# Performance work log

Hardware: AMD Instinct MI355X
Metric: run time of the kernel (lower is better)

Reference implementation:

```python
import jax, jax.numpy as jnp
import numpy as np

EPS = 1e-5
EMBED_DIM = 1024
CTX_DIM = 768
NUM_HEADS = 16
DH = EMBED_DIM // NUM_HEADS
# Faithful to torch source: embed_dim // num_heads ** 0.5 parses as embed_dim // (num_heads**0.5)
SCALE = EMBED_DIM // (NUM_HEADS ** 0.5)  # = 256.0


def ws_conv1x1(x, w, b, mask):
    # weight-standardized 1x1 conv1d: w [O, I, 1], x [B, I, T]
    w2 = w[..., 0]
    mu = jnp.mean(w2, axis=1, keepdims=True)
    var = jnp.var(w2, axis=1, keepdims=True)
    wn = (w2 - mu) * jax.lax.rsqrt(var + EPS)
    y = jnp.einsum('oi,bit->bot', wn, x) + b[None, :, None]
    if mask is not None:
        y = jnp.where(mask, y, 0.0)  # mask [B,1,T] bool
    return y


def layernorm(x, g, b):
    # normalize over last axis
    mu = jnp.mean(x, axis=-1, keepdims=True)
    var = jnp.var(x, axis=-1, keepdims=True)
    return (x - mu) * jax.lax.rsqrt(var + EPS) * g + b


def setup_inputs() -> dict:
    key = jax.random.key(0)
    ks = jax.random.split(key, 16)
    B, T, S = 4, 1024, 1024
    inp = {
        'x': jax.random.normal(ks[0], (B, EMBED_DIM, T), dtype=jnp.float32),
        'context': jax.random.normal(ks[1], (B, CTX_DIM, S), dtype=jnp.float32),
        'mask': jax.random.randint(ks[2], (B, 1, T), 0, 2).astype(bool),
        'mask_ctx': jax.random.randint(ks[3], (B, 1, S), 0, 2).astype(bool),
        'qw': jax.random.normal(ks[4], (EMBED_DIM, EMBED_DIM, 1), dtype=jnp.float32) * 0.02,
        'qb': jnp.zeros((EMBED_DIM,), jnp.float32),
        'kw': jax.random.normal(ks[5], (EMBED_DIM, CTX_DIM, 1), dtype=jnp.float32) * 0.02,
        'kb': jnp.zeros((EMBED_DIM,), jnp.float32),
        'vw': jax.random.normal(ks[6], (EMBED_DIM, CTX_DIM, 1), dtype=jnp.float32) * 0.02,
        'vb': jnp.zeros((EMBED_DIM,), jnp.float32),
        'ow': jax.random.normal(ks[7], (EMBED_DIM, EMBED_DIM, 1), dtype=jnp.float32) * 0.02,
        'ob': jnp.zeros((EMBED_DIM,), jnp.float32),
        'gq': jnp.ones((DH,), jnp.float32), 'bq': jnp.zeros((DH,), jnp.float32),
        'gk': jnp.ones((DH,), jnp.float32), 'bk': jnp.zeros((DH,), jnp.float32),
        'gv': jnp.ones((DH,), jnp.float32), 'bv': jnp.zeros((DH,), jnp.float32),
    }
    return inp


def reference(x, context, mask, mask_ctx, qw, qb, kw, kb, vw, vb, ow, ob, gq, bq, gk, bk, gv, bv):
    B, E, T = x.shape
    S = context.shape[-1]
    q = ws_conv1x1(x, qw, qb, mask)            # [B,E,T]
    k = ws_conv1x1(context, kw, kb, mask_ctx)  # [B,E,S]
    v = ws_conv1x1(context, vw, vb, mask_ctx)  # [B,E,S]
    # split heads -> [B,H,dh,L]
    q = q.reshape(B, NUM_HEADS, DH, T)
    k = k.reshape(B, NUM_HEADS, DH, S)
    v = v.reshape(B, NUM_HEADS, DH, S)
    # middle_norm: LayerNorm over dh (applied on transposed layout)
    q = jnp.swapaxes(layernorm(jnp.swapaxes(q, -1, -2), gq, bq), -1, -2)
    k = jnp.swapaxes(layernorm(jnp.swapaxes(k, -1, -2), gk, bk), -1, -2)
    v = jnp.swapaxes(layernorm(jnp.swapaxes(v, -1, -2), gv, bv), -1, -2)
    # scores: k^T @ q -> [B,H,S,T]
    scores = jnp.einsum('bhds,bhdt->bhst', k, q) / SCALE
    scores = jnp.where(mask[:, :, None, :], scores, -1e9)  # mask over query dim T
    scores = jax.nn.softmax(scores, axis=-1)               # softmax over T (as in source)
    scores = jnp.where(mask_ctx[:, :, :, None], scores, 0.0)
    out = jnp.einsum('bhds,bhst->bhdt', v, scores)          # v @ scores -> [B,H,dh,T]
    out = out.reshape(B, E, T)
    out = ws_conv1x1(out, ow, ob, mask) + x
    return out
```

## Files before the change

### kernel.cpp

```cpp
#include <hip/hip_runtime.h>

#define NB 4
#define TT 1024
#define SS 1024
#define EE 1024
#define CCH 768
#define NH 16
#define DHH 64
#define EPSF 1e-5f
#define QSCALE (1.4426950408889634f / 256.0f)

typedef unsigned short u16;
typedef __attribute__((ext_vector_type(8))) short short8;
typedef __attribute__((ext_vector_type(8))) unsigned short u16x8;
typedef __attribute__((ext_vector_type(4))) unsigned short u16x4;
typedef __attribute__((ext_vector_type(4))) float f32x4;

__device__ __forceinline__ u16 f2bu(float f) {
    union { float f; unsigned u; } x; x.f = f;
    unsigned r = x.u + 0x7fffu + ((x.u >> 16) & 1u);
    return (u16)(r >> 16);
}
__device__ __forceinline__ float bu2f(u16 u) {
    union { unsigned u; float f; } x; x.u = ((unsigned)u) << 16; return x.f;
}

#if __has_builtin(__builtin_amdgcn_exp2f)
#define EXP2(x) __builtin_amdgcn_exp2f(x)
#else
#define EXP2(x) exp2f(x)
#endif

#define MFMA16(a, b, c) __builtin_amdgcn_mfma_f32_16x16x32_bf16((a), (b), (c), 0, 0, 0)

__device__ __forceinline__ void gload16(const void* g, void* l) {
    __builtin_amdgcn_global_load_lds(
        (const __attribute__((address_space(1))) void*)g,
        (__attribute__((address_space(3))) void*)l, 16, 0, 0);
}

template<int R>
__device__ __forceinline__ void stage_tile(
    const u16* __restrict__ g, int ldg, u16* lds, int w, int lane) {
    constexpr int PW = R / 32;
    int r0 = lane >> 3;
    int cs = ((lane & 7) << 4) ^ (r0 << 4);
#pragma unroll
    for (int j = 0; j < PW; j++) {
        int inst = w * PW + j;
        const u16* src = g + (size_t)(inst * 8 + r0) * ldg + (cs >> 1);
        gload16(src, lds + inst * 512);
    }
}

__device__ __forceinline__ const u16* swz_ptr(const u16* tile, int row, int col) {
    int off = row * 128 + ((col * 2) ^ ((row & 7) << 4));
    return (const u16*)((const char*)tile + off);
}

#define PREP_WS_END   4096
#define PREP_SCAN_END (PREP_WS_END + 8)
#define PREP_TR_END   (PREP_SCAN_END + 1792)
#define PREP_FILL_END (PREP_TR_END + 4096)

__global__ __launch_bounds__(256) void prep(
    const float* __restrict__ qw, const float* __restrict__ kw,
    const float* __restrict__ vw, const float* __restrict__ ow,
    u16* __restrict__ wqn, u16* __restrict__ wkn,
    u16* __restrict__ wvn, u16* __restrict__ won,
    const float* __restrict__ x, const float* __restrict__ ctx,
    const int* __restrict__ mask, const int* __restrict__ mask_ctx,
    u16* __restrict__ xc, u16* __restrict__ cc,
    int* __restrict__ tIdx, int* __restrict__ sIdx,
    int* __restrict__ cntQ, int* __restrict__ cntK,
    float* __restrict__ outF) {
    __shared__ float tile[64][65];
    __shared__ int spos[64], smask[64], wtoti[4];
    __shared__ float sa[4], sb2[4], smean, srstd;
    int bid = blockIdx.x, tid = threadIdx.x;

    if (bid < PREP_WS_END) {
        int mat = bid >> 10, row = bid & 1023;
        const float* w = mat == 0 ? qw : (mat == 1 ? kw : (mat == 2 ? vw : ow));
        u16* wn = mat == 0 ? wqn : (mat == 1 ? wkn : (mat == 2 ? wvn : won));
        int I = (mat == 1 || mat == 2) ? CCH : EE;
        const float* wr = w + (size_t)row * I;
        int nv = I >> 8;
        float vals[4];
        float s = 0.f, s2 = 0.f;
        for (int j = 0; j < nv; j++) {
            float v = wr[tid + 256 * j];
            vals[j] = v; s += v; s2 += v * v;
        }
#pragma unroll
        for (int off = 32; off > 0; off >>= 1) { s += __shfl_down(s, off); s2 += __shfl_down(s2, off); }
        int wid = tid >> 6;
        if ((tid & 63) == 0) { sa[wid] = s; sb2[wid] = s2; }
        __syncthreads();
        if (tid == 0) {
            float ts = sa[0] + sa[1] + sa[2] + sa[3];
            float ts2 = sb2[0] + sb2[1] + sb2[2] + sb2[3];
            float mean = ts / (float)I;
            float var = ts2 / (float)I - mean * mean;
            smean = mean; srstd = rsqrtf(var + EPSF);
        }
        __syncthreads();
        float mean = smean, r = srstd;
        u16* wo = wn + (size_t)row * I;
        for (int j = 0; j < nv; j++) wo[tid + 256 * j] = f2bu((vals[j] - mean) * r);
        return;
    }
    if (bid < PREP_SCAN_END) {
        int t = bid - PREP_WS_END;
        int which = t & 1, b = t >> 1;
        const int* m = (which ? mask_ctx : mask) + b * 1024;
        int* idx = (which ? sIdx : tIdx) + b * 1024;
        int* cnt = (which ? cntK : cntQ) + b;
        int base = tid * 4;
        int v[4]; int s = 0;
#pragma unroll
        for (int i = 0; i < 4; i++) { v[i] = m[base + i] ? 1 : 0; s += v[i]; }
        int lane = tid & 63, wid = tid >> 6;
        int inc = s;
#pragma unroll
        for (int off = 1; off < 64; off <<= 1) {
            int o = __shfl_up(inc, off);
            if (lane >= off) inc += o;
        }
        if (lane == 63) wtoti[wid] = inc;
        __syncthreads();
        int woff = 0;
        for (int i = 0; i < wid; i++) woff += wtoti[i];
        int p = woff + inc - s;
#pragma unroll
        for (int i = 0; i < 4; i++) {
            if (v[i]) idx[p] = base + i;
            p += v[i];
        }
        if (tid == 255) *cnt = p;
        return;
    }
    if (bid < PREP_TR_END) {
        int t = bid - PREP_SCAN_END;
        int xb = t & 15; int rem = t >> 4;
        int yy = rem % 28, b = rem / 28;
        int mat = yy < 16 ? 0 : 1;
        int r0 = (mat == 0 ? yy : yy - 16) * 64;
        int R = mat == 0 ? EE : CCH;
        const float* in = mat == 0 ? x : ctx;
        const int* m = (mat == 0 ? mask : mask_ctx) + (size_t)b * 1024;
        u16* out = mat == 0 ? xc : cc;
        int c0 = xb * 64;
        const float* ip = in + (size_t)b * R * 1024;
        u16* op = out + (size_t)b * R * 1024;
#pragma unroll
        for (int mm = 0; mm < 16; mm++) {
            int id = tid + 256 * mm; int r = id >> 6, c = id & 63;
            tile[r][c] = ip[(size_t)(r0 + r) * 1024 + c0 + c];
        }
        int base = tid * 4;
        int v[4]; int s = 0;
#pragma unroll
        for (int i = 0; i < 4; i++) { v[i] = m[base + i] ? 1 : 0; s += v[i]; }
        int lane = tid & 63, wid = tid >> 6;
        int inc = s;
#pragma unroll
        for (int off = 1; off < 64; off <<= 1) {
            int o = __shfl_up(inc, off);
            if (lane >= off) inc += o;
        }
        if (lane == 63) wtoti[wid] = inc;
        __syncthreads();
        int woff = 0;
        for (int i = 0; i < wid; i++) woff += wtoti[i];
        int p = woff + inc - s;
#pragma unroll
        for (int i = 0; i < 4; i++) {
            int g = base + i;
            if (g >= c0 && g < c0 + 64) { spos[g - c0] = p; smask[g - c0] = v[i]; }
            p += v[i];
        }
        __syncthreads();
#pragma unroll
        for (int mm = 0; mm < 16; mm++) {
            int id = tid + 256 * mm; int rr = id >> 6, cc2 = id & 63;
            if (smask[rr])
                op[(size_t)spos[rr] * R + r0 + cc2] = f2bu(tile[cc2][rr]);
        }
        return;
    }
    {
        int f = bid - PREP_TR_END;
        int b = f >> 10, o = f & 1023;
        const float* xr = x + ((size_t)b * EE + o) * TT;
        float* orow = outF + ((size_t)b * EE + o) * TT;
        const int* mrow = mask + (size_t)b * TT;
        int4 mv = ((const int4*)mrow)[tid];
        float4 xv = ((const float4*)xr)[tid];
        int t4 = tid * 4;
        if (!mv.x) orow[t4 + 0] = xv.x;
        if (!mv.y) orow[t4 + 1] = xv.y;
        if (!mv.z) orow[t4 + 2] = xv.z;
        if (!mv.w) orow[t4 + 3] = xv.w;
    }
}

__device__ __forceinline__ void gemm_core(
    const u16* __restrict__ A, const u16* __restrict__ Bp, int I,
    int o0, int l0, u16 (*at)[128][64], u16 (*bt)[64][64], f32x4 (&acc)[4][2]) {
    int tid = threadIdx.x;
    int w = tid >> 6, lane = tid & 63, quad = lane >> 4, l16 = lane & 15;
    int wm = w & 1, wn = w >> 1;
    const u16* Ab = A + (size_t)o0 * I;
    const u16* Bb = Bp + (size_t)l0 * I;
    stage_tile<128>(Ab, I, &at[0][0][0], w, lane);
    stage_tile<64>(Bb, I, &bt[0][0][0], w, lane);
    __syncthreads();
    int cur = 0;
    for (int k0 = 0; k0 < I; k0 += 64, cur ^= 1) {
        int kn = k0 + 64;
        if (kn < I) {
            stage_tile<128>(Ab + kn, I, &at[cur ^ 1][0][0], w, lane);
            stage_tile<64>(Bb + kn, I, &bt[cur ^ 1][0][0], w, lane);
        }
#pragma unroll
        for (int ks = 0; ks < 64; ks += 32) {
            short8 af[4], bf[2];
#pragma unroll
            for (int i = 0; i < 4; i++)
                af[i] = *(const short8*)swz_ptr(&at[cur][0][0], wm * 64 + i * 16 + l16, ks + quad * 8);
#pragma unroll
            for (int j = 0; j < 2; j++)
                bf[j] = *(const short8*)swz_ptr(&bt[cur][0][0], wn * 32 + j * 16 + l16, ks + quad * 8);
#pragma unroll
            for (int mt = 0; mt < 4; mt++)
#pragma unroll
                for (int nt = 0; nt < 2; nt++)
                    acc[mt][nt] = MFMA16(af[mt], bf[nt], acc[mt][nt]);
        }
        __syncthreads();
    }
}

__global__ __launch_bounds__(256) void proj_qkv(
    const u16* __restrict__ wq, const u16* __restrict__ wk, const u16* __restrict__ wv,
    const u16* __restrict__ xc, const u16* __restrict__ cc,
    const float* __restrict__ qb, const float* __restrict__ kb, const float* __restrict__ vbi,
    const int* __restrict__ cntQ, const int* __restrict__ cntK,
    const float* __restrict__ gq, const float* __restrict__ bq,
    const float* __restrict__ gk, const float* __restrict__ bk,
    const float* __restrict__ gv, const float* __restrict__ bv,
    u16* __restrict__ qc, u16* __restrict__ kc, u16* __restrict__ vn) {
    int mat = blockIdx.x >> 3;
    int o0 = (blockIdx.x & 7) * 128;
    int l0 = blockIdx.y * 64;
    int b = blockIdx.z;
    int limit = (mat == 0) ? cntQ[b] : cntK[b];
    if (l0 >= limit) return;
    __shared__ u16 at[2][128][64];
    __shared__ u16 bt[2][64][64];
    __shared__ float sg[64], sbe[64], sbias[128];
    int tid = threadIdx.x;
    int w = tid >> 6, lane = tid & 63, quad = lane >> 4, l16 = lane & 15;
    int wm = w & 1, wn = w >> 1;
    const u16* A = mat == 0 ? wq : (mat == 1 ? wk : wv);
    const u16* BT = mat == 0 ? xc : cc;
    const float* bias = mat == 0 ? qb : (mat == 1 ? kb : vbi);
    int I = mat == 0 ? EE : CCH;
    if (tid < 64) {
        const float* gsrc = mat == 0 ? gq : (mat == 1 ? gk : gv);
        const float* bsrc = mat == 0 ? bq : (mat == 1 ? bk : bv);
        sg[tid] = gsrc[tid];
        sbe[tid] = bsrc[tid];
    }
    if (tid < 128) sbias[tid] = bias[o0 + tid];

    f32x4 acc[4][2] = {};
    gemm_core(A, BT + (size_t)b * 1024 * I, I, o0, l0, at, bt, acc);

    float scale = mat == 0 ? QSCALE : 1.0f;
    int h = (o0 >> 6) + wm;
    int bh = b * NH + h;
#pragma unroll
    for (int nt = 0; nt < 2; nt++) {
        int l = l0 + wn * 32 + nt * 16 + l16;
        float vbuf[16];
        float s = 0.f;
#pragma unroll
        for (int mt = 0; mt < 4; mt++)
#pragma unroll
            for (int reg = 0; reg < 4; reg++) {
                float v = acc[mt][nt][reg] + sbias[wm * 64 + mt * 16 + quad * 4 + reg];
                vbuf[mt * 4 + reg] = v; s += v;
            }
        s += __shfl_xor(s, 16); s += __shfl_xor(s, 32);
        float mean = s * (1.f / 64);
        float s2 = 0.f;
#pragma unroll
        for (int i = 0; i < 16; i++) { float dv = vbuf[i] - mean; s2 += dv * dv; }
        s2 += __shfl_xor(s2, 16); s2 += __shfl_xor(s2, 32);
        float r = rsqrtf(s2 * (1.f / 64) + EPSF);
        if (l < limit) {
            if (mat < 2) {
                u16* outT = mat == 0 ? qc : kc;
                u16* op = outT + ((size_t)bh * 1024 + l) * 64;
#pragma unroll
                for (int mt = 0; mt < 4; mt++) {
                    u16x4 pk;
#pragma unroll
                    for (int reg = 0; reg < 4; reg++) {
                        int d = mt * 16 + quad * 4 + reg;
                        pk[reg] = f2bu(((vbuf[mt * 4 + reg] - mean) * r * sg[d] + sbe[d]) * scale);
                    }
                    *(u16x4*)&op[mt * 16 + quad * 4] = pk;
                }
            } else {
#pragma unroll
                for (int mt = 0; mt < 4; mt++)
#pragma unroll
                    for (int reg = 0; reg < 4; reg++) {
                        int d = mt * 16 + quad * 4 + reg;
                        vn[((size_t)b * EE + h * 64 + d) * 1024 + l] =
                            f2bu((vbuf[mt * 4 + reg] - mean) * r * sg[d] + sbe[d]);
                    }
            }
        }
    }
}

__global__ __launch_bounds__(256) void attn_stats_mfma(
    const u16* __restrict__ qc, const u16* __restrict__ kc,
    const int* __restrict__ cntQ, const int* __restrict__ cntK,
    u16* __restrict__ vn, u16* __restrict__ P) {
    int s0 = blockIdx.x * 64, h = blockIdx.y, b = blockIdx.z;
    int Sc = cntK[b], Tc = cntQ[b];
    if (s0 >= Sc) return;
    __shared__ u16 kt[64][64];
    __shared__ u16 qt[2][64][64];
    __shared__ float lp[4][64];
    int tid = threadIdx.x;
    int w = tid >> 6, lane = tid & 63, quad = lane >> 4, l16 = lane & 15;
    int head = b * NH + h;
    const u16* kp = kc + (size_t)head * SS * DHH;
    const u16* qp = qc + (size_t)head * TT * DHH;
    u16* Pb = P + (size_t)head * TT * SS;
    stage_tile<64>(kp + (size_t)s0 * DHH, DHH, &kt[0][0], w, lane);
    stage_tile<64>(qp, DHH, &qt[0][0][0], w, lane);
    __syncthreads();
    float rl[4][4] = {};
    int cur = 0;
    for (int t0 = 0; t0 < Tc; t0 += 64, cur ^= 1) {
        if (t0 + 64 < Tc)
            stage_tile<64>(qp + (size_t)(t0 + 64) * DHH, DHH, &qt[cur ^ 1][0][0], w, lane);
        f32x4 acc[4] = {};
#pragma unroll
        for (int ks = 0; ks < 64; ks += 32) {
            short8 bf = *(const short8*)swz_ptr(&qt[cur][0][0], w * 16 + l16, ks + quad * 8);
#pragma unroll
            for (int mt = 0; mt < 4; mt++) {
                short8 af = *(const short8*)swz_ptr(&kt[0][0], mt * 16 + l16, ks + quad * 8);
                acc[mt] = MFMA16(af, bf, acc[mt]);
            }
        }
        int tcol = t0 + w * 16 + l16;
        int tok = tcol < Tc;
#pragma unroll
        for (int mt = 0; mt < 4; mt++) {
            u16x4 pk;
#pragma unroll
            for (int reg = 0; reg < 4; reg++) {
                int sl = s0 + mt * 16 + quad * 4 + reg;
                float e = EXP2(acc[mt][reg]);
                if (tok) rl[mt][reg] += e;
                pk[reg] = (sl < Sc) ? f2bu(e) : (u16)0;
            }
            *(u16x4*)&Pb[(size_t)tcol * SS + s0 + mt * 16 + quad * 4] = pk;
        }
        __syncthreads();
    }
#pragma unroll
    for (int mt = 0; mt < 4; mt++) {
#pragma unroll
        for (int reg = 0; reg < 4; reg++) {
            float v = rl[mt][reg];
            v += __shfl_xor(v, 1); v += __shfl_xor(v, 2);
            v += __shfl_xor(v, 4); v += __shfl_xor(v, 8);
            if (l16 == 0) lp[w][mt * 16 + quad * 4 + reg] = v;
        }
    }
    __syncthreads();
    {
        int so = tid & 63, dg = tid >> 6;
        int s = s0 + so;
        float lv = lp[0][so] + lp[1][so] + lp[2][so] + lp[3][so];
        float wsc = (lv > 0.f) ? (1.f / lv) : 0.f;
        u16* vrow = vn + ((size_t)b * EE + h * 64) * SS;
        int live = s < Sc;
#pragma unroll
        for (int i = 0; i < 16; i++) {
            int d = dg * 16 + i;
            size_t a = (size_t)d * SS + s;
            vrow[a] = live ? f2bu(bu2f(vrow[a]) * wsc) : (u16)0;
        }
    }
}

__global__ __launch_bounds__(256) void attn_pv_mfma(
    const u16* __restrict__ vn, const u16* __restrict__ P,
    const int* __restrict__ cntQ, const int* __restrict__ cntK,
    u16* __restrict__ ac) {
    int t0 = blockIdx.x * 64, h = blockIdx.y, b = blockIdx.z;
    int Tc = cntQ[b], Sc = cntK[b];
    if (t0 >= Tc) return;
    int Kc = (Sc + 63) & ~63;
    __shared__ u16 at[2][64][64];
    __shared__ u16 bt[2][64][64];
    __shared__ u16 pt[64][72];
    int tid = threadIdx.x;
    int w = tid >> 6, lane = tid & 63, quad = lane >> 4, l16 = lane & 15;
    int head = b * NH + h;
    const u16* vp = vn + ((size_t)head * DHH) * SS;
    const u16* Pb = P + (size_t)head * TT * SS + (size_t)t0 * SS;
    f32x4 oacc[4] = {};
    if (Kc > 0) {
        stage_tile<64>(vp, SS, &at[0][0][0], w, lane);
        stage_tile<64>(Pb, SS, &bt[0][0][0], w, lane);
        __syncthreads();
        int cur = 0;
        for (int k0 = 0; k0 < Kc; k0 += 64, cur ^= 1) {
            int kn = k0 + 64;
            if (kn < Kc) {
                stage_tile<64>(vp + kn, SS, &at[cur ^ 1][0][0], w, lane);
                stage_tile<64>(Pb + kn, SS, &bt[cur ^ 1][0][0], w, lane);
            }
#pragma unroll
            for (int ks = 0; ks < 64; ks += 32) {
                short8 bf = *(const short8*)swz_ptr(&bt[cur][0][0], w * 16 + l16, ks + quad * 8);
#pragma unroll
                for (int mt = 0; mt < 4; mt++) {
                    short8 af = *(const short8*)swz_ptr(&at[cur][0][0], mt * 16 + l16, ks + quad * 8);
                    oacc[mt] = MFMA16(af, bf, oacc[mt]);
                }
            }
            __syncthreads();
        }
    }
    int tl = w * 16 + l16;
#pragma unroll
    for (int mt = 0; mt < 4; mt++) {
        u16x4 pk;
#pragma unroll
        for (int reg = 0; reg < 4; reg++) pk[reg] = f2bu(oacc[mt][reg]);
        *(u16x4*)&pt[tl][mt * 16 + quad * 4] = pk;
    }
    __syncthreads();
#pragma unroll
    for (int i = 0; i < 2; i++) {
        int id = tid * 2 + i;
        int r = id >> 3, c = (id & 7) * 8;
        if (t0 + r < Tc)
            *(u16x8*)&ac[((size_t)b * TT + t0 + r) * EE + h * 64 + c] =
                *(const u16x8*)&pt[r][c];
    }
}

__global__ __launch_bounds__(256) void proj_o(
    const u16* __restrict__ won, const u16* __restrict__ ac,
    const float* __restrict__ obi, const int* __restrict__ tIdx,
    const int* __restrict__ cntQ, const float* __restrict__ x,
    float* __restrict__ out) {
    int o0 = blockIdx.x * 128, l0 = blockIdx.y * 64, b = blockIdx.z;
    int Tc = cntQ[b];
    if (l0 >= Tc) return;
    __shared__ u16 at[2][128][64];
    __shared__ u16 bt[2][64][64];
    __shared__ float sbias[128];
    __shared__ int stre[64];
    int tid = threadIdx.x;
    int w = tid >> 6, lane = tid & 63, quad = lane >> 4, l16 = lane & 15;
    int wm = w & 1, wn = w >> 1;
    if (tid < 128) sbias[tid] = obi[o0 + tid];
    if (tid < 64) stre[tid] = tIdx[(size_t)b * 1024 + l0 + tid];
    f32x4 acc[4][2] = {};
    gemm_core(won, ac + (size_t)b * TT * EE, EE, o0, l0, at, bt, acc);
#pragma unroll
    for (int nt = 0; nt < 2; nt++) {
        int lcol = wn * 32 + nt * 16 + l16;
        int l = l0 + lcol;
        if (l < Tc) {
            int treal = stre[lcol];
#pragma unroll
            for (int mt = 0; mt < 4; mt++)
#pragma unroll
                for (int reg = 0; reg < 4; reg++) {
                    int o = o0 + wm * 64 + mt * 16 + quad * 4 + reg;
                    size_t off = ((size_t)b * EE + o) * TT + treal;
                    out[off] = acc[mt][nt][reg] + sbias[wm * 64 + mt * 16 + quad * 4 + reg] + x[off];
                }
        }
    }
}

extern "C" void kernel_launch(void* const* d_in, const int* in_sizes, int n_in,
                              void* d_out, int out_size, void* d_ws, size_t ws_size,
                              hipStream_t stream) {
    const float* x        = (const float*)d_in[0];
    const float* ctx      = (const float*)d_in[1];
    const int*   mask     = (const int*)d_in[2];
    const int*   mask_ctx = (const int*)d_in[3];
    const float* qw  = (const float*)d_in[4];
    const float* qbi = (const float*)d_in[5];
    const float* kw  = (const float*)d_in[6];
    const float* kbi = (const float*)d_in[7];
    const float* vw  = (const float*)d_in[8];
    const float* vbi = (const float*)d_in[9];
    const float* ow  = (const float*)d_in[10];
    const float* obi = (const float*)d_in[11];
    const float* gq = (const float*)d_in[12];
    const float* bq = (const float*)d_in[13];
    const float* gk = (const float*)d_in[14];
    const float* bk = (const float*)d_in[15];
    const float* gv = (const float*)d_in[16];
    const float* bv = (const float*)d_in[17];

    u16* p = (u16*)d_ws;
    u16* wqn = p; p += (size_t)EE * EE;
    u16* wkn = p; p += (size_t)EE * CCH;
    u16* wvn = p; p += (size_t)EE * CCH;
    u16* won = p; p += (size_t)EE * EE;
    u16* xc  = p; p += (size_t)NB * TT * EE;
    u16* cc  = p; p += (size_t)NB * SS * CCH;
    u16* vn  = p; p += (size_t)NB * EE * SS;
    u16* qc  = p; p += (size_t)NB * NH * TT * DHH;
    u16* kc  = p; p += (size_t)NB * NH * SS * DHH;
    u16* ac  = p; p += (size_t)NB * TT * EE;
    u16* P   = p; p += (size_t)NB * NH * TT * SS;
    int* tIdx = (int*)p;
    int* sIdx = tIdx + NB * 1024;
    int* cntQ = sIdx + NB * 1024;
    int* cntK = cntQ + NB;

    prep<<<PREP_FILL_END, 256, 0, stream>>>(
        qw, kw, vw, ow, wqn, wkn, wvn, won, x, ctx, mask, mask_ctx,
        xc, cc, tIdx, sIdx, cntQ, cntK, (float*)d_out);

    proj_qkv<<<dim3(24, 16, NB), 256, 0, stream>>>(
        wqn, wkn, wvn, xc, cc, qbi, kbi, vbi, cntQ, cntK,
        gq, bq, gk, bk, gv, bv, qc, kc, vn);

    attn_stats_mfma<<<dim3(16, NH, NB), 256, 0, stream>>>(
        qc, kc, cntQ, cntK, vn, P);

    attn_pv_mfma<<<dim3(16, NH, NB), 256, 0, stream>>>(
        vn, P, cntQ, cntK, ac);

    proj_o<<<dim3(8, 16, NB), 256, 0, stream>>>(
        won, ac, obi, tIdx, cntQ, x, (float*)d_out);
}
```

Before: 227.1 us.

## Fuse attention stats, PV and output projection into one persistent kernel with grid barriers

Replaces three separate kernel launches (attention scores/exp, P·V, output projection) with a single kernel of 1024 blocks that runs the three phases back to back, separated by software grid barriers built on atomic counters. Shared memory is unioned across phases, and the output projection is retiled from 128x64 to 64x64 so it maps onto the same 1024-block grid. The goal is to remove launch gaps and tail effects between stages. In exchange it relies on all 1024 blocks being co-resident (launch bounds of 4 blocks per CU), pays for atomic spin barriers, and gives up the larger projection tile's data reuse.

```diff
diff --git a/kernel.cpp b/kernel.cpp
--- a/kernel.cpp
+++ b/kernel.cpp
@@ -10,6 +10,8 @@
 #define EPSF 1e-5f
 #define QSCALE (1.4426950408889634f / 256.0f)
 
+#define ATTN_BLKS 1024
+
 typedef unsigned short u16;
 typedef __attribute__((ext_vector_type(8))) short short8;
 typedef __attribute__((ext_vector_type(8))) unsigned short u16x8;
@@ -32,6 +34,21 @@
 #endif
 
 #define MFMA16(a, b, c) __builtin_amdgcn_mfma_f32_16x16x32_bf16((a), (b), (c), 0, 0, 0)
+
+__device__ unsigned int g_cnt[4];
+
+__device__ __forceinline__ void grid_barrier(int idx) {
+    __syncthreads();
+    if (threadIdx.x == 0) {
+        __threadfence();
+        unsigned ticket = atomicAdd(&g_cnt[idx], 1u);
+        unsigned target = (ticket / ATTN_BLKS + 1u) * ATTN_BLKS;
+        while (atomicAdd(&g_cnt[idx], 0u) < target)
+            __builtin_amdgcn_s_sleep(2);
+        __threadfence();
+    }
+    __syncthreads();
+}
 
 __device__ __forceinline__ void gload16(const void* g, void* l) {
     __builtin_amdgcn_global_load_lds(
@@ -328,175 +345,203 @@
     }
 }
 
-__global__ __launch_bounds__(256) void attn_stats_mfma(
+union ASMem {
+    struct {
+        u16 kt[64][64];
+        u16 qt[2][64][64];
+        float lp[4][64];
+    } st;
+    struct {
+        u16 at[2][64][64];
+        u16 bt[2][64][64];
+    } pv;
+    struct {
+        u16 at[2][64][64];
+        u16 bt[2][64][64];
+        float sbias[64];
+        int stre[64];
+    } po;
+};
+
+__global__ __launch_bounds__(256, 4) void attn_all(
     const u16* __restrict__ qc, const u16* __restrict__ kc,
+    u16* __restrict__ vn, u16* __restrict__ P, u16* __restrict__ ac,
+    const u16* __restrict__ won, const float* __restrict__ obi,
+    const int* __restrict__ tIdx,
     const int* __restrict__ cntQ, const int* __restrict__ cntK,
-    u16* __restrict__ vn, u16* __restrict__ P) {
-    int s0 = blockIdx.x * 64, h = blockIdx.y, b = blockIdx.z;
-    int Sc = cntK[b], Tc = cntQ[b];
-    if (s0 >= Sc) return;
-    __shared__ u16 kt[64][64];
-    __shared__ u16 qt[2][64][64];
-    __shared__ float lp[4][64];
-    int tid = threadIdx.x;
+    const float* __restrict__ x, float* __restrict__ out) {
+    __shared__ ASMem sm;
+    int bid = blockIdx.x, tid = threadIdx.x;
     int w = tid >> 6, lane = tid & 63, quad = lane >> 4, l16 = lane & 15;
-    int head = b * NH + h;
-    const u16* kp = kc + (size_t)head * SS * DHH;
-    const u16* qp = qc + (size_t)head * TT * DHH;
-    u16* Pb = P + (size_t)head * TT * SS;
-    stage_tile<64>(kp + (size_t)s0 * DHH, DHH, &kt[0][0], w, lane);
-    stage_tile<64>(qp, DHH, &qt[0][0][0], w, lane);
-    __syncthreads();
-    float rl[4][4] = {};
-    int cur = 0;
-    for (int t0 = 0; t0 < Tc; t0 += 64, cur ^= 1) {
-        if (t0 + 64 < Tc)
-            stage_tile<64>(qp + (size_t)(t0 + 64) * DHH, DHH, &qt[cur ^ 1][0][0], w, lane);
-        f32x4 acc[4] = {};
-#pragma unroll
-        for (int ks = 0; ks < 64; ks += 32) {
-            short8 bf = *(const short8*)swz_ptr(&qt[cur][0][0], w * 16 + l16, ks + quad * 8);
+    int gx = bid & 15, gy = (bid >> 4) & 15, b = bid >> 8;
+
+    {
+        int s0 = gx * 64, h = gy;
+        int Sc = cntK[b], Tc = cntQ[b];
+        if (s0 < Sc) {
+            int head = b * NH + h;
+            const u16* kp = kc + (size_t)head * SS * DHH;
+            const u16* qp = qc + (size_t)head * TT * DHH;
+            u16* Pb = P + (size_t)head * TT * SS;
+            stage_tile<64>(kp + (size_t)s0 * DHH, DHH, &sm.st.kt[0][0], w, lane);
+            stage_tile<64>(qp, DHH, &sm.st.qt[0][0][0], w, lane);
+            __syncthreads();
+            float rl[4][4] = {};
+            int cur = 0;
+            for (int t0 = 0; t0 < Tc; t0 += 64, cur ^= 1) {
+                if (t0 + 64 < Tc)
+                    stage_tile<64>(qp + (size_t)(t0 + 64) * DHH, DHH, &sm.st.qt[cur ^ 1][0][0], w, lane);
+                f32x4 acc[4] = {};
+#pragma unroll
+                for (int ks = 0; ks < 64; ks += 32) {
+                    short8 bf = *(const short8*)swz_ptr(&sm.st.qt[cur][0][0], w * 16 + l16, ks + quad * 8);
+#pragma unroll
+                    for (int mt = 0; mt < 4; mt++) {
+                        short8 af = *(const short8*)swz_ptr(&sm.st.kt[0][0], mt * 16 + l16, ks + quad * 8);
+                        acc[mt] = MFMA16(af, bf, acc[mt]);
+                    }
+                }
+                int tcol = t0 + w * 16 + l16;
+                int tok = tcol < Tc;
+#pragma unroll
+                for (int mt = 0; mt < 4; mt++) {
+                    u16x4 pk;
+#pragma unroll
+                    for (int reg = 0; reg < 4; reg++) {
+                        int sl = s0 + mt * 16 + quad * 4 + reg;
+                        float e = EXP2(acc[mt][reg]);
+                        if (tok) rl[mt][reg] += e;
+                        pk[reg] = (sl < Sc) ? f2bu(e) : (u16)0;
+                    }
+                    *(u16x4*)&Pb[(size_t)tcol * SS + s0 + mt * 16 + quad * 4] = pk;
+                }
+                __syncthreads();
+            }
 #pragma unroll
             for (int mt = 0; mt < 4; mt++) {
-                short8 af = *(const short8*)swz_ptr(&kt[0][0], mt * 16 + l16, ks + quad * 8);
-                acc[mt] = MFMA16(af, bf, acc[mt]);
-            }
-        }
-        int tcol = t0 + w * 16 + l16;
-        int tok = tcol < Tc;
-#pragma unroll
-        for (int mt = 0; mt < 4; mt++) {
-            u16x4 pk;
-#pragma unroll
-            for (int reg = 0; reg < 4; reg++) {
-                int sl = s0 + mt * 16 + quad * 4 + reg;
-                float e = EXP2(acc[mt][reg]);
-                if (tok) rl[mt][reg] += e;
-                pk[reg] = (sl < Sc) ? f2bu(e) : (u16)0;
-            }
-            *(u16x4*)&Pb[(size_t)tcol * SS + s0 + mt * 16 + quad * 4] = pk;
-        }
-        __syncthreads();
-    }
-#pragma unroll
-    for (int mt = 0; mt < 4; mt++) {
-#pragma unroll
-        for (int reg = 0; reg < 4; reg++) {
-            float v = rl[mt][reg];
-            v += __shfl_xor(v, 1); v += __shfl_xor(v, 2);
-            v += __shfl_xor(v, 4); v += __shfl_xor(v, 8);
-            if (l16 == 0) lp[w][mt * 16 + quad * 4 + reg] = v;
-        }
-    }
-    __syncthreads();
+#pragma unroll
+                for (int reg = 0; reg < 4; reg++) {
+                    float v = rl[mt][reg];
+                    v += __shfl_xor(v, 1); v += __shfl_xor(v, 2);
+                    v += __shfl_xor(v, 4); v += __shfl_xor(v, 8);
+                    if (l16 == 0) sm.st.lp[w][mt * 16 + quad * 4 + reg] = v;
+                }
+            }
+            __syncthreads();
+            {
+                int so = tid & 63, dg = tid >> 6;
+                int s = s0 + so;
+                float lv = sm.st.lp[0][so] + sm.st.lp[1][so] + sm.st.lp[2][so] + sm.st.lp[3][so];
+                float wsc = (lv > 0.f) ? (1.f / lv) : 0.f;
+                u16* vrow = vn + ((size_t)b * EE + h * 64) * SS;
+                int live = s < Sc;
+#pragma unroll
+                for (int i = 0; i < 16; i++) {
+                    int d = dg * 16 + i;
+                    size_t ad = (size_t)d * SS + s;
+                    vrow[ad] = live ? f2bu(bu2f(vrow[ad]) * wsc) : (u16)0;
+                }
+            }
+        }
+    }
+    grid_barrier(0);
     {
-        int so = tid & 63, dg = tid >> 6;
-        int s = s0 + so;
-        float lv = lp[0][so] + lp[1][so] + lp[2][so] + lp[3][so];
-        float wsc = (lv > 0.f) ? (1.f / lv) : 0.f;
-        u16* vrow = vn + ((size_t)b * EE + h * 64) * SS;
-        int live = s < Sc;
-#pragma unroll
-        for (int i = 0; i < 16; i++) {
-            int d = dg * 16 + i;
-            size_t a = (size_t)d * SS + s;
-            vrow[a] = live ? f2bu(bu2f(vrow[a]) * wsc) : (u16)0;
-        }
-    }
-}
-
-__global__ __launch_bounds__(256) void attn_pv_mfma(
-    const u16* __restrict__ vn, const u16* __restrict__ P,
-    const int* __restrict__ cntQ, const int* __restrict__ cntK,
-    u16* __restrict__ ac) {
-    int t0 = blockIdx.x * 64, h = blockIdx.y, b = blockIdx.z;
-    int Tc = cntQ[b], Sc = cntK[b];
-    if (t0 >= Tc) return;
-    int Kc = (Sc + 63) & ~63;
-    __shared__ u16 at[2][64][64];
-    __shared__ u16 bt[2][64][64];
-    __shared__ u16 pt[64][72];
-    int tid = threadIdx.x;
-    int w = tid >> 6, lane = tid & 63, quad = lane >> 4, l16 = lane & 15;
-    int head = b * NH + h;
-    const u16* vp = vn + ((size_t)head * DHH) * SS;
-    const u16* Pb = P + (size_t)head * TT * SS + (size_t)t0 * SS;
-    f32x4 oacc[4] = {};
-    if (Kc > 0) {
-        stage_tile<64>(vp, SS, &at[0][0][0], w, lane);
-        stage_tile<64>(Pb, SS, &bt[0][0][0], w, lane);
-        __syncthreads();
-        int cur = 0;
-        for (int k0 = 0; k0 < Kc; k0 += 64, cur ^= 1) {
-            int kn = k0 + 64;
-            if (kn < Kc) {
-                stage_tile<64>(vp + kn, SS, &at[cur ^ 1][0][0], w, lane);
-                stage_tile<64>(Pb + kn, SS, &bt[cur ^ 1][0][0], w, lane);
-            }
-#pragma unroll
-            for (int ks = 0; ks < 64; ks += 32) {
-                short8 bf = *(const short8*)swz_ptr(&bt[cur][0][0], w * 16 + l16, ks + quad * 8);
-#pragma unroll
-                for (int mt = 0; mt < 4; mt++) {
-                    short8 af = *(const short8*)swz_ptr(&at[cur][0][0], mt * 16 + l16, ks + quad * 8);
-                    oacc[mt] = MFMA16(af, bf, oacc[mt]);
-                }
+        int t0 = gx * 64, h = gy;
+        int Tc = cntQ[b], Sc = cntK[b];
+        if (t0 < Tc) {
+            int Kc = (Sc + 63) & ~63;
+            int head = b * NH + h;
+            const u16* vp = vn + ((size_t)head * DHH) * SS;
+            const u16* Pb = P + (size_t)head * TT * SS + (size_t)t0 * SS;
+            f32x4 oacc[4] = {};
+            if (Kc > 0) {
+                stage_tile<64>(vp, SS, &sm.pv.at[0][0][0], w, lane);
+                stage_tile<64>(Pb, SS, &sm.pv.bt[0][0][0], w, lane);
+                __syncthreads();
+                int cur = 0;
+                for (int k0 = 0; k0 < Kc; k0 += 64, cur ^= 1) {
+                    int kn = k0 + 64;
+                    if (kn < Kc) {
+                        stage_tile<64>(vp + kn, SS, &sm.pv.at[cur ^ 1][0][0], w, lane);
+                        stage_tile<64>(Pb + kn, SS, &sm.pv.bt[cur ^ 1][0][0], w, lane);
+                    }
+#pragma unroll
+                    for (int ks = 0; ks < 64; ks += 32) {
+                        short8 bf = *(const short8*)swz_ptr(&sm.pv.bt[cur][0][0], w * 16 + l16, ks + quad * 8);
+#pragma unroll
+                        for (int mt = 0; mt < 4; mt++) {
+                            short8 af = *(const short8*)swz_ptr(&sm.pv.at[cur][0][0], mt * 16 + l16, ks + quad * 8);
+                            oacc[mt] = MFMA16(af, bf, oacc[mt]);
+                        }
+                    }
+                    __syncthreads();
+                }
+            }
+            u16 (*pt)[72] = (u16(*)[72])&sm.pv.at[0][0][0];
+            int tl = w * 16 + l16;
+#pragma unroll
+            for (int mt = 0; mt < 4; mt++) {
+                u16x4 pk;
+#pragma unroll
+                for (int reg = 0; reg < 4; reg++) pk[reg] = f2bu(oacc[mt][reg]);
+                *(u16x4*)&pt[tl][mt * 16 + quad * 4] = pk;
             }
             __syncthreads();
-        }
-    }
-    int tl = w * 16 + l16;
-#pragma unroll
-    for (int mt = 0; mt < 4; mt++) {
-        u16x4 pk;
-#pragma unroll
-        for (int reg = 0; reg < 4; reg++) pk[reg] = f2bu(oacc[mt][reg]);
-        *(u16x4*)&pt[tl][mt * 16 + quad * 4] = pk;
-    }
-    __syncthreads();
-#pragma unroll
-    for (int i = 0; i < 2; i++) {
-        int id = tid * 2 + i;
-        int r = id >> 3, c = (id & 7) * 8;
-        if (t0 + r < Tc)
-            *(u16x8*)&ac[((size_t)b * TT + t0 + r) * EE + h * 64 + c] =
-                *(const u16x8*)&pt[r][c];
-    }
-}
-
-__global__ __launch_bounds__(256) void proj_o(
-    const u16* __restrict__ won, const u16* __restrict__ ac,
-    const float* __restrict__ obi, const int* __restrict__ tIdx,
-    const int* __restrict__ cntQ, const float* __restrict__ x,
-    float* __restrict__ out) {
-    int o0 = blockIdx.x * 128, l0 = blockIdx.y * 64, b = blockIdx.z;
-    int Tc = cntQ[b];
-    if (l0 >= Tc) return;
-    __shared__ u16 at[2][128][64];
-    __shared__ u16 bt[2][64][64];
-    __shared__ float sbias[128];
-    __shared__ int stre[64];
-    int tid = threadIdx.x;
-    int w = tid >> 6, lane = tid & 63, quad = lane >> 4, l16 = lane & 15;
-    int wm = w & 1, wn = w >> 1;
-    if (tid < 128) sbias[tid] = obi[o0 + tid];
-    if (tid < 64) stre[tid] = tIdx[(size_t)b * 1024 + l0 + tid];
-    f32x4 acc[4][2] = {};
-    gemm_core(won, ac + (size_t)b * TT * EE, EE, o0, l0, at, bt, acc);
-#pragma unroll
-    for (int nt = 0; nt < 2; nt++) {
-        int lcol = wn * 32 + nt * 16 + l16;
-        int l = l0 + lcol;
-        if (l < Tc) {
-            int treal = stre[lcol];
-#pragma unroll
-            for (int mt = 0; mt < 4; mt++)
-#pragma unroll
-                for (int reg = 0; reg < 4; reg++) {
-                    int o = o0 + wm * 64 + mt * 16 + quad * 4 + reg;
-                    size_t off = ((size_t)b * EE + o) * TT + treal;
-                    out[off] = acc[mt][nt][reg] + sbias[wm * 64 + mt * 16 + quad * 4 + reg] + x[off];
-                }
+#pragma unroll
+            for (int i = 0; i < 2; i++) {
+                int id = tid * 2 + i;
+                int r = id >> 3, c = (id & 7) * 8;
+                if (t0 + r < Tc)
+                    *(u16x8*)&ac[((size_t)b * TT + t0 + r) * EE + gy * 64 + c] =
+                        *(const u16x8*)&pt[r][c];
+            }
+        }
+    }
+    grid_barrier(1);
+    {
+        int o0 = gx * 64, l0 = gy * 64;
+        int Tc = cntQ[b];
+        if (l0 < Tc) {
+            if (tid < 64) {
+                sm.po.sbias[tid] = obi[o0 + tid];
+                sm.po.stre[tid] = tIdx[(size_t)b * 1024 + l0 + tid];
+            }
+            const u16* Ab = won + (size_t)o0 * EE;
+            const u16* Bb = ac + (size_t)b * TT * EE + (size_t)l0 * EE;
+            f32x4 acc[4] = {};
+            stage_tile<64>(Ab, EE, &sm.po.at[0][0][0], w, lane);
+            stage_tile<64>(Bb, EE, &sm.po.bt[0][0][0], w, lane);
+            __syncthreads();
+            int cur = 0;
+            for (int k0 = 0; k0 < EE; k0 += 64, cur ^= 1) {
+                int kn = k0 + 64;
+                if (kn < EE) {
+                    stage_tile<64>(Ab + kn, EE, &sm.po.at[cur ^ 1][0][0], w, lane);
+                    stage_tile<64>(Bb + kn, EE, &sm.po.bt[cur ^ 1][0][0], w, lane);
+                }
+#pragma unroll
+                for (int ks = 0; ks < 64; ks += 32) {
+                    short8 bf = *(const short8*)swz_ptr(&sm.po.bt[cur][0][0], w * 16 + l16, ks + quad * 8);
+#pragma unroll
+                    for (int mt = 0; mt < 4; mt++) {
+                        short8 af = *(const short8*)swz_ptr(&sm.po.at[cur][0][0], mt * 16 + l16, ks + quad * 8);
+                        acc[mt] = MFMA16(af, bf, acc[mt]);
+                    }
+                }
+                __syncthreads();
+            }
+            int l = l0 + w * 16 + l16;
+            if (l < Tc) {
+                int treal = sm.po.stre[w * 16 + l16];
+#pragma unroll
+                for (int mt = 0; mt < 4; mt++)
+#pragma unroll
+                    for (int reg = 0; reg < 4; reg++) {
+                        int o = o0 + mt * 16 + quad * 4 + reg;
+                        size_t off = ((size_t)b * EE + o) * TT + treal;
+                        out[off] = acc[mt][reg] + sm.po.sbias[mt * 16 + quad * 4 + reg] + x[off];
+                    }
+            }
         }
     }
 }
@@ -548,12 +593,6 @@
         wqn, wkn, wvn, xc, cc, qbi, kbi, vbi, cntQ, cntK,
         gq, bq, gk, bk, gv, bv, qc, kc, vn);
 
-    attn_stats_mfma<<<dim3(16, NH, NB), 256, 0, stream>>>(
-        qc, kc, cntQ, cntK, vn, P);
-
-    attn_pv_mfma<<<dim3(16, NH, NB), 256, 0, stream>>>(
-        vn, P, cntQ, cntK, ac);
-
-    proj_o<<<dim3(8, 16, NB), 256, 0, stream>>>(
-        won, ac, obi, tIdx, cntQ, x, (float*)d_out);
-}
+    attn_all<<<dim3(ATTN_BLKS), dim3(256), 0, stream>>>(
+        qc, kc, vn, P, ac, won, obi, tIdx, cntQ, cntK, x, (float*)d_out);
+}
```

Result: slower. 421.3 us (+85.5%).

## Replace LDS staging with direct global-to-register MFMA fragment loads in attention and output projection

Applied to the files above, without the earlier changes.

Three kernels (attn_stats, attn_pv, proj_o) drop their shared-memory tiles and barriers. Each lane now loads its MFMA fragments straight from global memory into registers, with a two-stage software prefetch. proj_o moves to 64-row output tiles, which doubles its grid, and attn_pv writes each output element directly instead of going through an LDS transpose. This removes LDS traffic and sync overhead, but gives up cross-wave reuse of tiles in shared memory, adds redundant global/L2 reads, and leaves stores less coalesced.

```diff
diff --git a/kernel.cpp b/kernel.cpp
--- a/kernel.cpp
+++ b/kernel.cpp
@@ -328,15 +328,13 @@
     }
 }
 
-__global__ __launch_bounds__(256) void attn_stats_mfma(
+__global__ __launch_bounds__(256) void attn_stats(
     const u16* __restrict__ qc, const u16* __restrict__ kc,
     const int* __restrict__ cntQ, const int* __restrict__ cntK,
     u16* __restrict__ vn, u16* __restrict__ P) {
     int s0 = blockIdx.x * 64, h = blockIdx.y, b = blockIdx.z;
     int Sc = cntK[b], Tc = cntQ[b];
     if (s0 >= Sc) return;
-    __shared__ u16 kt[64][64];
-    __shared__ u16 qt[2][64][64];
     __shared__ float lp[4][64];
     int tid = threadIdx.x;
     int w = tid >> 6, lane = tid & 63, quad = lane >> 4, l16 = lane & 15;
@@ -344,40 +342,54 @@
     const u16* kp = kc + (size_t)head * SS * DHH;
     const u16* qp = qc + (size_t)head * TT * DHH;
     u16* Pb = P + (size_t)head * TT * SS;
-    stage_tile<64>(kp + (size_t)s0 * DHH, DHH, &kt[0][0], w, lane);
-    stage_tile<64>(qp, DHH, &qt[0][0][0], w, lane);
-    __syncthreads();
+
+    short8 af[4][2];
+#pragma unroll
+    for (int mt = 0; mt < 4; mt++) {
+        const u16* kr = kp + (size_t)(s0 + mt * 16 + l16) * DHH + quad * 8;
+        af[mt][0] = *(const short8*)kr;
+        af[mt][1] = *(const short8*)(kr + 32);
+    }
+    const u16* qr = qp + (size_t)(w * 16 + l16) * DHH + quad * 8;
     float rl[4][4] = {};
-    int cur = 0;
-    for (int t0 = 0; t0 < Tc; t0 += 64, cur ^= 1) {
-        if (t0 + 64 < Tc)
-            stage_tile<64>(qp + (size_t)(t0 + 64) * DHH, DHH, &qt[cur ^ 1][0][0], w, lane);
-        f32x4 acc[4] = {};
-#pragma unroll
-        for (int ks = 0; ks < 64; ks += 32) {
-            short8 bf = *(const short8*)swz_ptr(&qt[cur][0][0], w * 16 + l16, ks + quad * 8);
-#pragma unroll
-            for (int mt = 0; mt < 4; mt++) {
-                short8 af = *(const short8*)swz_ptr(&kt[0][0], mt * 16 + l16, ks + quad * 8);
-                acc[mt] = MFMA16(af, bf, acc[mt]);
-            }
-        }
-        int tcol = t0 + w * 16 + l16;
-        int tok = tcol < Tc;
-#pragma unroll
-        for (int mt = 0; mt < 4; mt++) {
-            u16x4 pk;
-#pragma unroll
-            for (int reg = 0; reg < 4; reg++) {
-                int sl = s0 + mt * 16 + quad * 4 + reg;
-                float e = EXP2(acc[mt][reg]);
-                if (tok) rl[mt][reg] += e;
-                pk[reg] = (sl < Sc) ? f2bu(e) : (u16)0;
-            }
-            *(u16x4*)&Pb[(size_t)tcol * SS + s0 + mt * 16 + quad * 4] = pk;
-        }
-        __syncthreads();
-    }
+
+#define LOADQ(B, tb) { B[0] = *(const short8*)(qr + (size_t)(tb) * DHH); \
+                       B[1] = *(const short8*)(qr + (size_t)(tb) * DHH + 32); }
+#define SBODY(B, tb) { \
+        f32x4 acc[4] = {}; \
+        _Pragma("unroll") \
+        for (int mt = 0; mt < 4; mt++) { \
+            acc[mt] = MFMA16(af[mt][0], B[0], acc[mt]); \
+            acc[mt] = MFMA16(af[mt][1], B[1], acc[mt]); \
+        } \
+        int tcol = (tb) + w * 16 + l16; \
+        int tok = tcol < Tc; \
+        _Pragma("unroll") \
+        for (int mt = 0; mt < 4; mt++) { \
+            u16x4 pk; \
+            _Pragma("unroll") \
+            for (int reg = 0; reg < 4; reg++) { \
+                int sl = s0 + mt * 16 + quad * 4 + reg; \
+                float e = EXP2(acc[mt][reg]); \
+                if (tok) rl[mt][reg] += e; \
+                pk[reg] = (sl < Sc) ? f2bu(e) : (u16)0; \
+            } \
+            *(u16x4*)&Pb[(size_t)tcol * SS + s0 + mt * 16 + quad * 4] = pk; \
+        } }
+
+    short8 B0[2], B1[2];
+    LOADQ(B0, 0);
+    for (int t0 = 0; t0 < Tc; t0 += 128) {
+        if (t0 + 64 < Tc) LOADQ(B1, t0 + 64);
+        SBODY(B0, t0);
+        if (t0 + 64 < Tc) {
+            if (t0 + 128 < Tc) LOADQ(B0, t0 + 128);
+            SBODY(B1, t0 + 64);
+        }
+    }
+#undef LOADQ
+#undef SBODY
+
 #pragma unroll
     for (int mt = 0; mt < 4; mt++) {
 #pragma unroll
@@ -399,13 +411,13 @@
 #pragma unroll
         for (int i = 0; i < 16; i++) {
             int d = dg * 16 + i;
-            size_t a = (size_t)d * SS + s;
-            vrow[a] = live ? f2bu(bu2f(vrow[a]) * wsc) : (u16)0;
-        }
-    }
-}
-
-__global__ __launch_bounds__(256) void attn_pv_mfma(
+            size_t ad = (size_t)d * SS + s;
+            vrow[ad] = live ? f2bu(bu2f(vrow[ad]) * wsc) : (u16)0;
+        }
+    }
+}
+
+__global__ __launch_bounds__(256) void attn_pv(
     const u16* __restrict__ vn, const u16* __restrict__ P,
     const int* __restrict__ cntQ, const int* __restrict__ cntK,
     u16* __restrict__ ac) {
@@ -413,55 +425,52 @@
     int Tc = cntQ[b], Sc = cntK[b];
     if (t0 >= Tc) return;
     int Kc = (Sc + 63) & ~63;
-    __shared__ u16 at[2][64][64];
-    __shared__ u16 bt[2][64][64];
-    __shared__ u16 pt[64][72];
     int tid = threadIdx.x;
     int w = tid >> 6, lane = tid & 63, quad = lane >> 4, l16 = lane & 15;
     int head = b * NH + h;
-    const u16* vp = vn + ((size_t)head * DHH) * SS;
-    const u16* Pb = P + (size_t)head * TT * SS + (size_t)t0 * SS;
-    f32x4 oacc[4] = {};
-    if (Kc > 0) {
-        stage_tile<64>(vp, SS, &at[0][0][0], w, lane);
-        stage_tile<64>(Pb, SS, &bt[0][0][0], w, lane);
-        __syncthreads();
-        int cur = 0;
-        for (int k0 = 0; k0 < Kc; k0 += 64, cur ^= 1) {
-            int kn = k0 + 64;
-            if (kn < Kc) {
-                stage_tile<64>(vp + kn, SS, &at[cur ^ 1][0][0], w, lane);
-                stage_tile<64>(Pb + kn, SS, &bt[cur ^ 1][0][0], w, lane);
-            }
-#pragma unroll
-            for (int ks = 0; ks < 64; ks += 32) {
-                short8 bf = *(const short8*)swz_ptr(&bt[cur][0][0], w * 16 + l16, ks + quad * 8);
-#pragma unroll
-                for (int mt = 0; mt < 4; mt++) {
-                    short8 af = *(const short8*)swz_ptr(&at[cur][0][0], mt * 16 + l16, ks + quad * 8);
-                    oacc[mt] = MFMA16(af, bf, oacc[mt]);
-                }
-            }
-            __syncthreads();
-        }
-    }
-    int tl = w * 16 + l16;
-#pragma unroll
-    for (int mt = 0; mt < 4; mt++) {
-        u16x4 pk;
-#pragma unroll
-        for (int reg = 0; reg < 4; reg++) pk[reg] = f2bu(oacc[mt][reg]);
-        *(u16x4*)&pt[tl][mt * 16 + quad * 4] = pk;
-    }
-    __syncthreads();
-#pragma unroll
-    for (int i = 0; i < 2; i++) {
-        int id = tid * 2 + i;
-        int r = id >> 3, c = (id & 7) * 8;
-        if (t0 + r < Tc)
-            *(u16x8*)&ac[((size_t)b * TT + t0 + r) * EE + h * 64 + c] =
-                *(const u16x8*)&pt[r][c];
-    }
+    const u16* Pb = P + (size_t)head * TT * SS;
+    const u16* a0 = Pb + (size_t)(t0 +  0 + l16) * SS + quad * 8;
+    const u16* a1 = Pb + (size_t)(t0 + 16 + l16) * SS + quad * 8;
+    const u16* a2 = Pb + (size_t)(t0 + 32 + l16) * SS + quad * 8;
+    const u16* a3 = Pb + (size_t)(t0 + 48 + l16) * SS + quad * 8;
+    const u16* br = vn + ((size_t)b * EE + h * 64 + w * 16 + l16) * SS + quad * 8;
+
+#define LOADF(A, B, k0) { \
+        A[0][0] = *(const short8*)(a0 + (k0));      A[0][1] = *(const short8*)(a0 + (k0) + 32); \
+        A[1][0] = *(const short8*)(a1 + (k0));      A[1][1] = *(const short8*)(a1 + (k0) + 32); \
+        A[2][0] = *(const short8*)(a2 + (k0));      A[2][1] = *(const short8*)(a2 + (k0) + 32); \
+        A[3][0] = *(const short8*)(a3 + (k0));      A[3][1] = *(const short8*)(a3 + (k0) + 32); \
+        B[0]    = *(const short8*)(br + (k0));      B[1]    = *(const short8*)(br + (k0) + 32); }
+#define MF8(A, B) { \
+        _Pragma("unroll") \
+        for (int mt = 0; mt < 4; mt++) { \
+            acc[mt] = MFMA16(A[mt][0], B[0], acc[mt]); \
+            acc[mt] = MFMA16(A[mt][1], B[1], acc[mt]); \
+        } }
+
+    short8 A0[4][2], B0[2], A1[4][2], B1[2];
+    f32x4 acc[4] = {};
+    LOADF(A0, B0, 0);
+    for (int k0 = 0; k0 < Kc; k0 += 128) {
+        if (k0 + 64 < Kc) LOADF(A1, B1, k0 + 64);
+        MF8(A0, B0);
+        if (k0 + 64 < Kc) {
+            if (k0 + 128 < Kc) LOADF(A0, B0, k0 + 128);
+            MF8(A1, B1);
+        }
+    }
+#undef LOADF
+#undef MF8
+
+    int d = w * 16 + l16;
+#pragma unroll
+    for (int mt = 0; mt < 4; mt++)
+#pragma unroll
+        for (int reg = 0; reg < 4; reg++) {
+            int t = t0 + mt * 16 + quad * 4 + reg;
+            if (t < Tc)
+                ac[((size_t)b * TT + t) * EE + h * 64 + d] = f2bu(acc[mt][reg]);
+        }
 }
 
 __global__ __launch_bounds__(256) void proj_o(
@@ -469,35 +478,53 @@
     const float* __restrict__ obi, const int* __restrict__ tIdx,
     const int* __restrict__ cntQ, const float* __restrict__ x,
     float* __restrict__ out) {
-    int o0 = blockIdx.x * 128, l0 = blockIdx.y * 64, b = blockIdx.z;
+    int o0 = blockIdx.x * 64, l0 = blockIdx.y * 64, b = blockIdx.z;
     int Tc = cntQ[b];
     if (l0 >= Tc) return;
-    __shared__ u16 at[2][128][64];
-    __shared__ u16 bt[2][64][64];
-    __shared__ float sbias[128];
-    __shared__ int stre[64];
     int tid = threadIdx.x;
     int w = tid >> 6, lane = tid & 63, quad = lane >> 4, l16 = lane & 15;
-    int wm = w & 1, wn = w >> 1;
-    if (tid < 128) sbias[tid] = obi[o0 + tid];
-    if (tid < 64) stre[tid] = tIdx[(size_t)b * 1024 + l0 + tid];
-    f32x4 acc[4][2] = {};
-    gemm_core(won, ac + (size_t)b * TT * EE, EE, o0, l0, at, bt, acc);
-#pragma unroll
-    for (int nt = 0; nt < 2; nt++) {
-        int lcol = wn * 32 + nt * 16 + l16;
-        int l = l0 + lcol;
-        if (l < Tc) {
-            int treal = stre[lcol];
-#pragma unroll
-            for (int mt = 0; mt < 4; mt++)
-#pragma unroll
-                for (int reg = 0; reg < 4; reg++) {
-                    int o = o0 + wm * 64 + mt * 16 + quad * 4 + reg;
-                    size_t off = ((size_t)b * EE + o) * TT + treal;
-                    out[off] = acc[mt][nt][reg] + sbias[wm * 64 + mt * 16 + quad * 4 + reg] + x[off];
-                }
-        }
+    const u16* a0 = won + (size_t)(o0 +  0 + l16) * EE + quad * 8;
+    const u16* a1 = won + (size_t)(o0 + 16 + l16) * EE + quad * 8;
+    const u16* a2 = won + (size_t)(o0 + 32 + l16) * EE + quad * 8;
+    const u16* a3 = won + (size_t)(o0 + 48 + l16) * EE + quad * 8;
+    const u16* br = ac + ((size_t)b * TT + l0 + w * 16 + l16) * EE + quad * 8;
+
+#define LOADF(A, B, k0) { \
+        A[0][0] = *(const short8*)(a0 + (k0));      A[0][1] = *(const short8*)(a0 + (k0) + 32); \
+        A[1][0] = *(const short8*)(a1 + (k0));      A[1][1] = *(const short8*)(a1 + (k0) + 32); \
+        A[2][0] = *(const short8*)(a2 + (k0));      A[2][1] = *(const short8*)(a2 + (k0) + 32); \
+        A[3][0] = *(const short8*)(a3 + (k0));      A[3][1] = *(const short8*)(a3 + (k0) + 32); \
+        B[0]    = *(const short8*)(br + (k0));      B[1]    = *(const short8*)(br + (k0) + 32); }
+#define MF8(A, B) { \
+        _Pragma("unroll") \
+        for (int mt = 0; mt < 4; mt++) { \
+            acc[mt] = MFMA16(A[mt][0], B[0], acc[mt]); \
+            acc[mt] = MFMA16(A[mt][1], B[1], acc[mt]); \
+        } }
+
+    short8 A0[4][2], B0[2], A1[4][2], B1[2];
+    f32x4 acc[4] = {};
+    LOADF(A0, B0, 0);
+    for (int k0 = 0; k0 < EE; k0 += 128) {
+        LOADF(A1, B1, k0 + 64);
+        MF8(A0, B0);
+        if (k0 + 128 < EE) LOADF(A0, B0, k0 + 128);
+        MF8(A1, B1);
+    }
+#undef LOADF
+#undef MF8
+
+    int l = l0 + w * 16 + l16;
+    if (l < Tc) {
+        int treal = tIdx[(size_t)b * 1024 + l];
+#pragma unroll
+        for (int mt = 0; mt < 4; mt++)
+#pragma unroll
+            for (int reg = 0; reg < 4; reg++) {
+                int o = o0 + mt * 16 + quad * 4 + reg;
+                size_t off = ((size_t)b * EE + o) * TT + treal;
+                out[off] = acc[mt][reg] + obi[o] + x[off];
+            }
     }
 }
 
@@ -548,12 +575,12 @@
         wqn, wkn, wvn, xc, cc, qbi, kbi, vbi, cntQ, cntK,
         gq, bq, gk, bk, gv, bv, qc, kc, vn);
 
-    attn_stats_mfma<<<dim3(16, NH, NB), 256, 0, stream>>>(
+    attn_stats<<<dim3(16, NH, NB), 256, 0, stream>>>(
         qc, kc, cntQ, cntK, vn, P);
 
-    attn_pv_mfma<<<dim3(16, NH, NB), 256, 0, stream>>>(
+    attn_pv<<<dim3(16, NH, NB), 256, 0, stream>>>(
         vn, P, cntQ, cntK, ac);
 
-    proj_o<<<dim3(8, 16, NB), 256, 0, stream>>>(
+    proj_o<<<dim3(16, 16, NB), 256, 0, stream>>>(
         won, ac, obi, tIdx, cntQ, x, (float*)d_out);
 }
```

After: 306.1 us. +34.8%, slower.
